# Kernel tuning notes

Measured on AMD Instinct MI355X. Metric: run time of the kernel, lower is better.

The kernel has to match this reference:

```python
import jax, jax.numpy as jnp
import numpy as np

N = 50000        # nodes
E = 800000       # edges (avg degree 16)
F = 64           # node_feature
H = 128          # dim_h
C = 10           # num_classes
G = 512          # graphs in batch
BN_EPS = 1e-5


def setup_inputs() -> dict:
    key = jax.random.key(0)
    ks = iter(jax.random.split(key, 40))
    inp = {}
    inp['x'] = jax.random.normal(next(ks), (N, F), dtype=jnp.float32)
    inp['edge_index'] = jax.random.randint(next(ks), (2, E), 0, N, dtype=jnp.int32)
    inp['batch'] = jnp.sort(jax.random.randint(next(ks), (N,), 0, G, dtype=jnp.int32))
    # GINConv MLP params (Linear, BatchNorm1d(eval), ReLU, Linear, ReLU) x3
    in_dims = [F, H, H]
    for i in range(1, 4):
        d_in = in_dims[i - 1]
        inp[f'c{i}_w1'] = jax.random.normal(next(ks), (d_in, H), dtype=jnp.float32) * 0.05
        inp[f'c{i}_b1'] = jnp.zeros((H,), dtype=jnp.float32)
        inp[f'c{i}_g'] = jnp.ones((H,), dtype=jnp.float32)
        inp[f'c{i}_be'] = jnp.zeros((H,), dtype=jnp.float32)
        inp[f'c{i}_m'] = jax.random.normal(next(ks), (H,), dtype=jnp.float32) * 0.01
        inp[f'c{i}_v'] = jax.random.uniform(next(ks), (H,), dtype=jnp.float32) + 0.5
        inp[f'c{i}_w2'] = jax.random.normal(next(ks), (H, H), dtype=jnp.float32) * 0.05
        inp[f'c{i}_b2'] = jnp.zeros((H,), dtype=jnp.float32)
    inp['lin1_w'] = jax.random.normal(next(ks), (3 * H, 3 * H), dtype=jnp.float32) * 0.05
    inp['lin1_b'] = jnp.zeros((3 * H,), dtype=jnp.float32)
    inp['lin2_w'] = jax.random.normal(next(ks), (3 * H, C), dtype=jnp.float32) * 0.05
    inp['lin2_b'] = jnp.zeros((C,), dtype=jnp.float32)
    return inp


def _mlp(h, w1, b1, g, be, m, v, w2, b2):
    h = h @ w1 + b1
    h = (h - m) * jax.lax.rsqrt(v + BN_EPS) * g + be  # BatchNorm1d (eval)
    h = jax.nn.relu(h)
    return jax.nn.relu(h @ w2 + b2)


def _gin_conv(x, src, dst, w1, b1, g, be, m, v, w2, b2):
    # GINConv, eps=0: MLP(x_i + sum_{j->i} x_j)
    agg = jax.ops.segment_sum(x[src], dst, num_segments=N)
    return _mlp(x + agg, w1, b1, g, be, m, v, w2, b2)


def reference(x, edge_index, batch,
              c1_w1, c1_b1, c1_g, c1_be, c1_m, c1_v, c1_w2, c1_b2,
              c2_w1, c2_b1, c2_g, c2_be, c2_m, c2_v, c2_w2, c2_b2,
              c3_w1, c3_b1, c3_g, c3_be, c3_m, c3_v, c3_w2, c3_b2,
              lin1_w, lin1_b, lin2_w, lin2_b):
    src, dst = edge_index[0], edge_index[1]
    h1 = _gin_conv(x, src, dst, c1_w1, c1_b1, c1_g, c1_be, c1_m, c1_v, c1_w2, c1_b2)
    h2 = _gin_conv(h1, src, dst, c2_w1, c2_b1, c2_g, c2_be, c2_m, c2_v, c2_w2, c2_b2)
    h3 = _gin_conv(h2, src, dst, c3_w1, c3_b1, c3_g, c3_be, c3_m, c3_v, c3_w2, c3_b2)
    p1 = jax.ops.segment_sum(h1, batch, num_segments=G)  # global_add_pool
    p2 = jax.ops.segment_sum(h2, batch, num_segments=G)
    p3 = jax.ops.segment_sum(h3, batch, num_segments=G)
    h = jnp.concatenate((p1, p2, p3), axis=1)  # [G, 3H]
    h = jax.nn.relu(h @ lin1_w + lin1_b)
    # dropout is identity in eval mode
    h = h @ lin2_w + lin2_b
    return jax.nn.log_softmax(h, axis=1)
```

## Files before the change

### kernel.cpp

```cpp
#include <hip/hip_runtime.h>
#include <math.h>
#include <stdint.h>

static constexpr int NN = 50000;
static constexpr int NE = 800000;
static constexpr int NG = 512;
static constexpr int NB = (NN + 255) / 256;
static constexpr float BNEPS = 1e-5f;

typedef __bf16 bf16x8 __attribute__((ext_vector_type(8)));
typedef __bf16 bf16x2 __attribute__((ext_vector_type(2)));
typedef float f32x4 __attribute__((ext_vector_type(4)));

__device__ __forceinline__ uint32_t pack_bf16(float x, float y) {
    bf16x2 v; v[0] = (__bf16)x; v[1] = (__bf16)y;
    return __builtin_bit_cast(uint32_t, v);
}
__device__ __forceinline__ float2 unpack_bf16(uint32_t u) {
    bf16x2 v = __builtin_bit_cast(bf16x2, u);
    return make_float2((float)v[0], (float)v[1]);
}


__global__ void degree_kernel(const int* __restrict__ dst, int* __restrict__ deg,
                              uint16_t* __restrict__ rank) {
    int e = blockIdx.x * blockDim.x + threadIdx.x;
    if (e < NE) rank[e] = (uint16_t)atomicAdd(&deg[dst[e]], 1);
}

__global__ __launch_bounds__(256) void blocksum_kernel(const int* __restrict__ deg,
                                                       int* __restrict__ bsum) {
    int i = blockIdx.x * 256 + threadIdx.x;
    int v = (i < NN) ? deg[i] : 0;
#pragma unroll
    for (int off = 32; off; off >>= 1) v += __shfl_down(v, off, 64);
    __shared__ int s[4];
    if ((threadIdx.x & 63) == 0) s[threadIdx.x >> 6] = v;
    __syncthreads();
    if (threadIdx.x == 0) bsum[blockIdx.x] = s[0] + s[1] + s[2] + s[3];
}

__global__ __launch_bounds__(256) void scanb_kernel(const int* __restrict__ bsum,
                                                    int* __restrict__ bscan,
                                                    int* __restrict__ row_ptr) {
    __shared__ int s[256];
    int t = threadIdx.x;
    int v = (t < NB) ? bsum[t] : 0;
    s[t] = v;
    __syncthreads();
    for (int off = 1; off < 256; off <<= 1) {
        int u = (t >= off) ? s[t - off] : 0;
        __syncthreads();
        s[t] += u;
        __syncthreads();
    }
    if (t < NB) bscan[t] = s[t] - v;
    if (t == NB - 1) row_ptr[NN] = s[t];
}

__global__ __launch_bounds__(256) void scanfinal_kernel(const int* __restrict__ deg,
                                                        const int* __restrict__ bscan,
                                                        int* __restrict__ row_ptr) {
    __shared__ int s[256];
    int t = threadIdx.x;
    int i = blockIdx.x * 256 + t;
    int v = (i < NN) ? deg[i] : 0;
    s[t] = v;
    __syncthreads();
    for (int off = 1; off < 256; off <<= 1) {
        int u = (t >= off) ? s[t - off] : 0;
        __syncthreads();
        s[t] += u;
        __syncthreads();
    }
    if (i < NN) row_ptr[i] = bscan[blockIdx.x] + s[t] - v;
}

__global__ void fill_kernel(const int* __restrict__ src, const int* __restrict__ dst,
                            const int* __restrict__ row_ptr, const uint16_t* __restrict__ rank,
                            uint16_t* __restrict__ cols) {
    int e = blockIdx.x * blockDim.x + threadIdx.x;
    if (e < NE) cols[row_ptr[dst[e]] + (int)rank[e]] = (uint16_t)src[e];
}


__global__ void prep_kernel(const float* __restrict__ x, __bf16* __restrict__ xb,
                            const float* s0, const float* s1, const float* s2,
                            const float* s3, const float* s4, const float* s5,
                            const float* s6,
                            __bf16* d0, __bf16* d1, __bf16* d2,
                            __bf16* d3, __bf16* d4, __bf16* d5, __bf16* d6) {
    int i = blockIdx.x * blockDim.x + threadIdx.x;
    if (i < 800000) {
        float4 v = *(const float4*)&x[i * 4];
        xb[i * 4 + 0] = (__bf16)v.x;
        xb[i * 4 + 1] = (__bf16)v.y;
        xb[i * 4 + 2] = (__bf16)v.z;
        xb[i * 4 + 3] = (__bf16)v.w;
        return;
    }
    int j = i - 800000;
    if (j < 8192) {
        int l = j;           int n = l / 64,  k = l % 64;  d0[l] = (__bf16)s0[k * 128 + n];
    } else if (j < 24576) {
        int l = j - 8192;    int n = l / 128, k = l % 128; d1[l] = (__bf16)s1[k * 128 + n];
    } else if (j < 40960) {
        int l = j - 24576;   int n = l / 128, k = l % 128; d2[l] = (__bf16)s2[k * 128 + n];
    } else if (j < 57344) {
        int l = j - 40960;   int n = l / 128, k = l % 128; d3[l] = (__bf16)s3[k * 128 + n];
    } else if (j < 73728) {
        int l = j - 57344;   int n = l / 128, k = l % 128; d4[l] = (__bf16)s4[k * 128 + n];
    } else if (j < 90112) {
        int l = j - 73728;   int n = l / 128, k = l % 128; d5[l] = (__bf16)s5[k * 128 + n];
    } else if (j < 237568) {
        int l = j - 90112;   int n = l / 384, k = l % 384; d6[l] = (__bf16)s6[k * 384 + n];
    }
}


__global__ __launch_bounds__(512) void gather64_kernel(const __bf16* __restrict__ in,
                                                       const int* __restrict__ row_ptr,
                                                       const uint16_t* __restrict__ cols,
                                                       __bf16* __restrict__ agg) {
    int node = blockIdx.x * 8 + (threadIdx.x >> 6);
    int lane = threadIdx.x & 63;
    if (node >= NN) return;
    int beg = row_ptr[node], end = row_ptr[node + 1];
    float acc0 = (float)in[(size_t)node * 64 + lane];
    float acc1 = 0.f;
    int i = beg;
    for (; i + 8 <= end; i += 8) {
        int c0 = cols[i], c1 = cols[i + 1], c2 = cols[i + 2], c3 = cols[i + 3];
        int c4 = cols[i + 4], c5 = cols[i + 5], c6 = cols[i + 6], c7 = cols[i + 7];
        float v0 = (float)in[(size_t)c0 * 64 + lane];
        float v1 = (float)in[(size_t)c1 * 64 + lane];
        float v2 = (float)in[(size_t)c2 * 64 + lane];
        float v3 = (float)in[(size_t)c3 * 64 + lane];
        float v4 = (float)in[(size_t)c4 * 64 + lane];
        float v5 = (float)in[(size_t)c5 * 64 + lane];
        float v6 = (float)in[(size_t)c6 * 64 + lane];
        float v7 = (float)in[(size_t)c7 * 64 + lane];
        acc0 += (v0 + v1) + (v2 + v3);
        acc1 += (v4 + v5) + (v6 + v7);
    }
    for (; i < end; ++i) acc0 += (float)in[(size_t)cols[i] * 64 + lane];
    agg[(size_t)node * 64 + lane] = (__bf16)(acc0 + acc1);
}

__global__ __launch_bounds__(512) void gather128_kernel(const __bf16* __restrict__ in,
                                                        const int* __restrict__ row_ptr,
                                                        const uint16_t* __restrict__ cols,
                                                        __bf16* __restrict__ agg) {
    int node = blockIdx.x * 8 + (threadIdx.x >> 6);
    int lane = threadIdx.x & 63;
    if (node >= NN) return;
    const uint32_t* inu = (const uint32_t*)in;
    uint32_t* aggu = (uint32_t*)agg;
    int beg = row_ptr[node], end = row_ptr[node + 1];
    float2 a0 = unpack_bf16(inu[(size_t)node * 64 + lane]);
    float2 a1 = make_float2(0.f, 0.f);
    int i = beg;
    for (; i + 8 <= end; i += 8) {
        int c0 = cols[i], c1 = cols[i + 1], c2 = cols[i + 2], c3 = cols[i + 3];
        int c4 = cols[i + 4], c5 = cols[i + 5], c6 = cols[i + 6], c7 = cols[i + 7];
        uint32_t u0 = inu[(size_t)c0 * 64 + lane];
        uint32_t u1 = inu[(size_t)c1 * 64 + lane];
        uint32_t u2 = inu[(size_t)c2 * 64 + lane];
        uint32_t u3 = inu[(size_t)c3 * 64 + lane];
        uint32_t u4 = inu[(size_t)c4 * 64 + lane];
        uint32_t u5 = inu[(size_t)c5 * 64 + lane];
        uint32_t u6 = inu[(size_t)c6 * 64 + lane];
        uint32_t u7 = inu[(size_t)c7 * 64 + lane];
        float2 v0 = unpack_bf16(u0), v1 = unpack_bf16(u1);
        float2 v2 = unpack_bf16(u2), v3 = unpack_bf16(u3);
        float2 v4 = unpack_bf16(u4), v5 = unpack_bf16(u5);
        float2 v6 = unpack_bf16(u6), v7 = unpack_bf16(u7);
        a0.x += (v0.x + v1.x) + (v2.x + v3.x);
        a0.y += (v0.y + v1.y) + (v2.y + v3.y);
        a1.x += (v4.x + v5.x) + (v6.x + v7.x);
        a1.y += (v4.y + v5.y) + (v6.y + v7.y);
    }
    for (; i < end; ++i) {
        float2 v = unpack_bf16(inu[(size_t)cols[i] * 64 + lane]);
        a0.x += v.x; a0.y += v.y;
    }
    aggu[(size_t)node * 64 + lane] = pack_bf16(a0.x + a1.x, a0.y + a1.y);
}


template <int K, bool WOUT>
__global__ __launch_bounds__(512, 1) void mlp_mfma_kernel(
    const __bf16* __restrict__ agg,
    const __bf16* __restrict__ w1t,
    const float* __restrict__ b1,
    const float* __restrict__ g, const float* __restrict__ be,
    const float* __restrict__ m, const float* __restrict__ v,
    const __bf16* __restrict__ w2t,
    const float* __restrict__ b2,
    __bf16* __restrict__ out,
    const int* __restrict__ batch,
    float* __restrict__ p,
    int col_off)
{
    constexpr int KP = K + 8;
    constexpr int KP2 = 136;
    __shared__ alignas(16) __bf16 sA[64 * KP];
    __shared__ alignas(16) __bf16 sW1[128 * KP];
    __shared__ alignas(16) __bf16 sW2[128 * KP2];
    __shared__ alignas(16) __bf16 sT[64 * KP2];
    __shared__ alignas(16) __bf16 sOut[64 * KP2];
    __shared__ int sBatch[64];

    int tid = threadIdx.x;
    int wid = tid >> 6, lane = tid & 63;
    int wr = wid >> 1, wc = wid & 1;
    int l15 = lane & 15, lq = lane >> 4;
    int rowbase = blockIdx.x * 64;

    for (int idx = tid; idx < 64 * (K / 8); idx += 512) {
        int r = idx / (K / 8), kc = idx % (K / 8);
        int n = rowbase + r;
        uint4 val = make_uint4(0, 0, 0, 0);
        if (n < NN) val = *(const uint4*)&agg[(size_t)n * K + kc * 8];
        *(uint4*)&sA[r * KP + kc * 8] = val;
    }
    for (int idx = tid; idx < 128 * (K / 8); idx += 512) {
        int n = idx / (K / 8), kc = idx % (K / 8);
        *(uint4*)&sW1[n * KP + kc * 8] = *(const uint4*)&w1t[n * K + kc * 8];
    }
    for (int idx = tid; idx < 128 * 16; idx += 512) {
        int n = idx >> 4, kc = idx & 15;
        *(uint4*)&sW2[n * KP2 + kc * 8] = *(const uint4*)&w2t[n * 128 + kc * 8];
    }
    if (tid < 64) {
        int n = rowbase + tid;
        sBatch[tid] = (n < NN) ? batch[n] : -1;
    }
    __syncthreads();

    f32x4 acc[4] = {};
#pragma unroll
    for (int ks = 0; ks < K / 32; ++ks) {
        bf16x8 a = *(const bf16x8*)&sA[(wr * 16 + l15) * KP + ks * 32 + lq * 8];
#pragma unroll
        for (int nf = 0; nf < 4; ++nf) {
            bf16x8 b = *(const bf16x8*)&sW1[(wc * 64 + nf * 16 + l15) * KP + ks * 32 + lq * 8];
            acc[nf] = __builtin_amdgcn_mfma_f32_16x16x32_bf16(a, b, acc[nf], 0, 0, 0);
        }
    }
#pragma unroll
    for (int nf = 0; nf < 4; ++nf) {
        int c = wc * 64 + nf * 16 + l15;
        float sc = g[c] * rsqrtf(v[c] + BNEPS);
        float sh = be[c] + (b1[c] - m[c]) * sc;
#pragma unroll
        for (int r = 0; r < 4; ++r) {
            int row = wr * 16 + lq * 4 + r;
            float t = fmaxf(acc[nf][r] * sc + sh, 0.f);
            sT[row * KP2 + c] = (__bf16)t;
        }
    }
    __syncthreads();

    f32x4 acc2[4] = {};
#pragma unroll
    for (int ks = 0; ks < 4; ++ks) {
        bf16x8 a = *(const bf16x8*)&sT[(wr * 16 + l15) * KP2 + ks * 32 + lq * 8];
#pragma unroll
        for (int nf = 0; nf < 4; ++nf) {
            bf16x8 b = *(const bf16x8*)&sW2[(wc * 64 + nf * 16 + l15) * KP2 + ks * 32 + lq * 8];
            acc2[nf] = __builtin_amdgcn_mfma_f32_16x16x32_bf16(a, b, acc2[nf], 0, 0, 0);
        }
    }
#pragma unroll
    for (int nf = 0; nf < 4; ++nf) {
        int c = wc * 64 + nf * 16 + l15;
        float bb = b2[c];
#pragma unroll
        for (int r = 0; r < 4; ++r) {
            int row = wr * 16 + lq * 4 + r;
            float o = fmaxf(acc2[nf][r] + bb, 0.f);
            sOut[row * KP2 + c] = (__bf16)o;
        }
    }
    __syncthreads();

    if constexpr (WOUT) {
        for (int idx = tid; idx < 64 * 16; idx += 512) {
            int r = idx >> 4, kc = idx & 15;
            int n = rowbase + r;
            if (n < NN)
                *(uint4*)&out[(size_t)n * 128 + kc * 8] = *(const uint4*)&sOut[r * KP2 + kc * 8];
        }
    }

    {
        int f = tid & 127;
        int chunk = tid >> 7;
        float pacc = 0.f;
        int cur = -1;
#pragma unroll
        for (int i = 0; i < 16; ++i) {
            int row = chunk * 16 + i;
            int b = sBatch[row];
            if (b < 0) break;
            if (b != cur) {
                if (cur >= 0) atomicAdd(&p[cur * 384 + col_off + f], pacc);
                pacc = 0.f;
                cur = b;
            }
            pacc += (float)sOut[row * KP2 + f];
        }
        if (cur >= 0) atomicAdd(&p[cur * 384 + col_off + f], pacc);
    }
}


__global__ __launch_bounds__(512, 1) void head1_kernel(const float* __restrict__ p,
                                                       const __bf16* __restrict__ lin1t,
                                                       const float* __restrict__ b1,
                                                       float* __restrict__ hrelu) {
    constexpr int KPA = 392;
    constexpr int KPW = 136;
    __shared__ alignas(16) __bf16 sA[64 * KPA];
    __shared__ alignas(16) __bf16 sW[128 * KPW];

    int tid = threadIdx.x;
    int wid = tid >> 6, lane = tid & 63;
    int wr = wid >> 1, wc = wid & 1;
    int l15 = lane & 15, lq = lane >> 4;
    int rowbase = blockIdx.x * 64;
    int colbase = blockIdx.y * 128;

    for (int idx = tid; idx < 64 * 48; idx += 512) {
        int r = idx / 48, kc = idx % 48;
        const float* srcp = &p[(rowbase + r) * 384 + kc * 8];
        float4 v0 = *(const float4*)srcp;
        float4 v1 = *(const float4*)(srcp + 4);
        bf16x8 o;
        o[0] = (__bf16)v0.x; o[1] = (__bf16)v0.y; o[2] = (__bf16)v0.z; o[3] = (__bf16)v0.w;
        o[4] = (__bf16)v1.x; o[5] = (__bf16)v1.y; o[6] = (__bf16)v1.z; o[7] = (__bf16)v1.w;
        *(bf16x8*)&sA[r * KPA + kc * 8] = o;
    }

    f32x4 acc[4] = {};
#pragma unroll
    for (int kchunk = 0; kchunk < 3; ++kchunk) {
        for (int idx = tid; idx < 128 * 16; idx += 512) {
            int n = idx >> 4, kc = idx & 15;
            *(uint4*)&sW[n * KPW + kc * 8] =
                *(const uint4*)&lin1t[(colbase + n) * 384 + kchunk * 128 + kc * 8];
        }
        __syncthreads();
#pragma unroll
        for (int ks = 0; ks < 4; ++ks) {
            bf16x8 a = *(const bf16x8*)&sA[(wr * 16 + l15) * KPA + kchunk * 128 + ks * 32 + lq * 8];
#pragma unroll
            for (int nf = 0; nf < 4; ++nf) {
                bf16x8 b = *(const bf16x8*)&sW[(wc * 64 + nf * 16 + l15) * KPW + ks * 32 + lq * 8];
                acc[nf] = __builtin_amdgcn_mfma_f32_16x16x32_bf16(a, b, acc[nf], 0, 0, 0);
            }
        }
        __syncthreads();
    }
#pragma unroll
    for (int nf = 0; nf < 4; ++nf) {
        int col = colbase + wc * 64 + nf * 16 + l15;
        float bb = b1[col];
#pragma unroll
        for (int r = 0; r < 4; ++r) {
            int row = rowbase + wr * 16 + lq * 4 + r;
            hrelu[row * 384 + col] = fmaxf(acc[nf][r] + bb, 0.f);
        }
    }
}


__global__ __launch_bounds__(256) void head2_kernel(const float* __restrict__ hrelu,
                                                    const float* __restrict__ w2,
                                                    const float* __restrict__ b2,
                                                    float* __restrict__ out) {
    int wid = threadIdx.x >> 6, lane = threadIdx.x & 63;
    int gidx = blockIdx.x * 4 + wid;
    const float* hr = &hrelu[gidx * 384 + lane * 6];
    float h[6];
#pragma unroll
    for (int u = 0; u < 6; ++u) h[u] = hr[u];
    float logit[10];
#pragma unroll
    for (int c = 0; c < 10; ++c) {
        float s = 0.f;
#pragma unroll
        for (int u = 0; u < 6; ++u) s = fmaf(h[u], w2[(lane * 6 + u) * 10 + c], s);
#pragma unroll
        for (int off = 32; off; off >>= 1) s += __shfl_xor(s, off, 64);
        logit[c] = s + b2[c];
    }
    float mx = logit[0];
#pragma unroll
    for (int c = 1; c < 10; ++c) mx = fmaxf(mx, logit[c]);
    float se = 0.f;
#pragma unroll
    for (int c = 0; c < 10; ++c) se += expf(logit[c] - mx);
    float lse = logf(se);
    float val = 0.f;
#pragma unroll
    for (int c = 0; c < 10; ++c) if (lane == c) val = logit[c];
    if (lane < 10) out[gidx * 10 + lane] = val - mx - lse;
}


static inline char* align_up(char* ptr, size_t a) {
    return (char*)(((uintptr_t)ptr + a - 1) & ~(uintptr_t)(a - 1));
}

extern "C" void kernel_launch(void* const* d_in, const int* in_sizes, int n_in,
                              void* d_out, int out_size, void* d_ws, size_t ws_size,
                              hipStream_t stream) {
    const float* x = (const float*)d_in[0];
    const int* ei = (const int*)d_in[1];
    const int* batch = (const int*)d_in[2];
    const float* c_w1[3], *c_b1[3], *c_g[3], *c_be[3], *c_m[3], *c_v[3], *c_w2[3], *c_b2[3];
    for (int i = 0; i < 3; ++i) {
        int base = 3 + i * 8;
        c_w1[i] = (const float*)d_in[base + 0];
        c_b1[i] = (const float*)d_in[base + 1];
        c_g[i]  = (const float*)d_in[base + 2];
        c_be[i] = (const float*)d_in[base + 3];
        c_m[i]  = (const float*)d_in[base + 4];
        c_v[i]  = (const float*)d_in[base + 5];
        c_w2[i] = (const float*)d_in[base + 6];
        c_b2[i] = (const float*)d_in[base + 7];
    }
    const float* lin1_w = (const float*)d_in[27];
    const float* lin1_b = (const float*)d_in[28];
    const float* lin2_w = (const float*)d_in[29];
    const float* lin2_b = (const float*)d_in[30];
    const int* src = ei;
    const int* dst = ei + NE;
    float* out = (float*)d_out;

    char* ws = (char*)d_ws;
    __bf16* xb  = (__bf16*)ws; ws = align_up(ws + (size_t)NN * 64 * 2, 256);
    __bf16* agg = (__bf16*)ws; ws = align_up(ws + (size_t)NN * 128 * 2, 256);
    __bf16* hA  = (__bf16*)ws; ws = align_up(ws + (size_t)NN * 128 * 2, 256);
    __bf16* hB  = (__bf16*)ws; ws = align_up(ws + (size_t)NN * 128 * 2, 256);
    float* p    = (float*)ws;  ws = align_up(ws + (size_t)NG * 384 * 4, 256);
    float* hrelu = (float*)ws; ws = align_up(ws + (size_t)NG * 384 * 4, 256);
    int* csr_row = (int*)ws;   ws = align_up(ws + (size_t)(NN + 1) * 4, 256);
    int* cursor  = (int*)ws;   ws = align_up(ws + (size_t)NN * 4, 256);
    uint16_t* csr_src = (uint16_t*)ws; ws = align_up(ws + (size_t)NE * 2, 256);
    uint16_t* rank    = (uint16_t*)ws; ws = align_up(ws + (size_t)NE * 2, 256);
    int* bsum    = (int*)ws;   ws = align_up(ws + (size_t)NB * 4, 256);
    int* bscan   = (int*)ws;   ws = align_up(ws + (size_t)NB * 4, 256);
    __bf16* w1t[3]; __bf16* w2t[3];
    for (int i = 0; i < 3; ++i) {
        int K = (i == 0) ? 64 : 128;
        w1t[i] = (__bf16*)ws; ws = align_up(ws + (size_t)128 * K * 2, 256);
        w2t[i] = (__bf16*)ws; ws = align_up(ws + (size_t)128 * 128 * 2, 256);
    }
    __bf16* lin1t = (__bf16*)ws; ws = align_up(ws + (size_t)384 * 384 * 2, 256);

    hipMemsetAsync(cursor, 0, (size_t)NN * 4, stream);
    degree_kernel<<<(NE + 255) / 256, 256, 0, stream>>>(dst, cursor, rank);
    blocksum_kernel<<<NB, 256, 0, stream>>>(cursor, bsum);
    scanb_kernel<<<1, 256, 0, stream>>>(bsum, bscan, csr_row);
    scanfinal_kernel<<<NB, 256, 0, stream>>>(cursor, bscan, csr_row);
    fill_kernel<<<(NE + 255) / 256, 256, 0, stream>>>(src, dst, csr_row, rank, csr_src);
    hipMemsetAsync(p, 0, (size_t)NG * 384 * 4, stream);

    prep_kernel<<<(800000 + 237568 + 255) / 256, 256, 0, stream>>>(
        x, xb,
        c_w1[0], c_w1[1], c_w1[2], c_w2[0], c_w2[1], c_w2[2], lin1_w,
        w1t[0], w1t[1], w1t[2], w2t[0], w2t[1], w2t[2], lin1t);

    const int GATHER_BLOCKS = (NN + 7) / 8;
    const int MLP_BLOCKS = (NN + 63) / 64;

    gather64_kernel<<<GATHER_BLOCKS, 512, 0, stream>>>(xb, csr_row, csr_src, agg);
    mlp_mfma_kernel<64, true><<<MLP_BLOCKS, 512, 0, stream>>>(agg, w1t[0], c_b1[0], c_g[0], c_be[0],
                                                              c_m[0], c_v[0], w2t[0], c_b2[0], hA,
                                                              batch, p, 0);

    gather128_kernel<<<GATHER_BLOCKS, 512, 0, stream>>>(hA, csr_row, csr_src, agg);
    mlp_mfma_kernel<128, true><<<MLP_BLOCKS, 512, 0, stream>>>(agg, w1t[1], c_b1[1], c_g[1], c_be[1],
                                                               c_m[1], c_v[1], w2t[1], c_b2[1], hB,
                                                               batch, p, 128);

    gather128_kernel<<<GATHER_BLOCKS, 512, 0, stream>>>(hB, csr_row, csr_src, agg);
    mlp_mfma_kernel<128, false><<<MLP_BLOCKS, 512, 0, stream>>>(agg, w1t[2], c_b1[2], c_g[2], c_be[2],
                                                                c_m[2], c_v[2], w2t[2], c_b2[2], nullptr,
                                                                batch, p, 256);

    head1_kernel<<<dim3(8, 3), 512, 0, stream>>>(p, lin1t, lin1_b, hrelu);
    head2_kernel<<<128, 256, 0, stream>>>(hrelu, lin2_w, lin2_b, out);
}
```

Measured before the change: 273.2 us.

## Split gather into column passes with 16-lane groups per node

Replaces the per-wave-per-node gather kernels with one templated kernel. Each 16-lane subgroup handles one node and a 64-byte column slice, and blockIdx.y selects which slice. The intent is to shrink the working set of source rows touched at once so it fits in cache better, and to fit more nodes per wave, which cuts wasted lanes on low-degree nodes. In exchange, the CSR row pointers and column indices are reread once per column pass, the accesses are narrower, and the inner loop is unrolled 4 instead of 8, so fewer loads are in flight.

```diff
diff --git a/kernel.cpp b/kernel.cpp
--- a/kernel.cpp
+++ b/kernel.cpp
@@ -118,73 +118,39 @@
 }
 
 
-__global__ __launch_bounds__(512) void gather64_kernel(const __bf16* __restrict__ in,
-                                                       const int* __restrict__ row_ptr,
-                                                       const uint16_t* __restrict__ cols,
-                                                       __bf16* __restrict__ agg) {
-    int node = blockIdx.x * 8 + (threadIdx.x >> 6);
-    int lane = threadIdx.x & 63;
+template <int DWPR>
+__global__ __launch_bounds__(512) void gather_pass_kernel(const __bf16* __restrict__ in,
+                                                          const int* __restrict__ row_ptr,
+                                                          const uint16_t* __restrict__ cols,
+                                                          __bf16* __restrict__ agg) {
+    int wid = threadIdx.x >> 6;
+    int sub = (threadIdx.x & 63) >> 4;
+    int l16 = threadIdx.x & 15;
+    int node = (blockIdx.x * 8 + wid) * 4 + sub;
     if (node >= NN) return;
-    int beg = row_ptr[node], end = row_ptr[node + 1];
-    float acc0 = (float)in[(size_t)node * 64 + lane];
-    float acc1 = 0.f;
-    int i = beg;
-    for (; i + 8 <= end; i += 8) {
-        int c0 = cols[i], c1 = cols[i + 1], c2 = cols[i + 2], c3 = cols[i + 3];
-        int c4 = cols[i + 4], c5 = cols[i + 5], c6 = cols[i + 6], c7 = cols[i + 7];
-        float v0 = (float)in[(size_t)c0 * 64 + lane];
-        float v1 = (float)in[(size_t)c1 * 64 + lane];
-        float v2 = (float)in[(size_t)c2 * 64 + lane];
-        float v3 = (float)in[(size_t)c3 * 64 + lane];
-        float v4 = (float)in[(size_t)c4 * 64 + lane];
-        float v5 = (float)in[(size_t)c5 * 64 + lane];
-        float v6 = (float)in[(size_t)c6 * 64 + lane];
-        float v7 = (float)in[(size_t)c7 * 64 + lane];
-        acc0 += (v0 + v1) + (v2 + v3);
-        acc1 += (v4 + v5) + (v6 + v7);
-    }
-    for (; i < end; ++i) acc0 += (float)in[(size_t)cols[i] * 64 + lane];
-    agg[(size_t)node * 64 + lane] = (__bf16)(acc0 + acc1);
-}
-
-__global__ __launch_bounds__(512) void gather128_kernel(const __bf16* __restrict__ in,
-                                                        const int* __restrict__ row_ptr,
-                                                        const uint16_t* __restrict__ cols,
-                                                        __bf16* __restrict__ agg) {
-    int node = blockIdx.x * 8 + (threadIdx.x >> 6);
-    int lane = threadIdx.x & 63;
-    if (node >= NN) return;
+    int off = blockIdx.y * 16 + l16;
     const uint32_t* inu = (const uint32_t*)in;
     uint32_t* aggu = (uint32_t*)agg;
     int beg = row_ptr[node], end = row_ptr[node + 1];
-    float2 a0 = unpack_bf16(inu[(size_t)node * 64 + lane]);
+    float2 a0 = unpack_bf16(inu[(size_t)node * DWPR + off]);
     float2 a1 = make_float2(0.f, 0.f);
     int i = beg;
-    for (; i + 8 <= end; i += 8) {
+    for (; i + 4 <= end; i += 4) {
         int c0 = cols[i], c1 = cols[i + 1], c2 = cols[i + 2], c3 = cols[i + 3];
-        int c4 = cols[i + 4], c5 = cols[i + 5], c6 = cols[i + 6], c7 = cols[i + 7];
-        uint32_t u0 = inu[(size_t)c0 * 64 + lane];
-        uint32_t u1 = inu[(size_t)c1 * 64 + lane];
-        uint32_t u2 = inu[(size_t)c2 * 64 + lane];
-        uint32_t u3 = inu[(size_t)c3 * 64 + lane];
-        uint32_t u4 = inu[(size_t)c4 * 64 + lane];
-        uint32_t u5 = inu[(size_t)c5 * 64 + lane];
-        uint32_t u6 = inu[(size_t)c6 * 64 + lane];
-        uint32_t u7 = inu[(size_t)c7 * 64 + lane];
+        uint32_t u0 = inu[(size_t)c0 * DWPR + off];
+        uint32_t u1 = inu[(size_t)c1 * DWPR + off];
+        uint32_t u2 = inu[(size_t)c2 * DWPR + off];
+        uint32_t u3 = inu[(size_t)c3 * DWPR + off];
         float2 v0 = unpack_bf16(u0), v1 = unpack_bf16(u1);
         float2 v2 = unpack_bf16(u2), v3 = unpack_bf16(u3);
-        float2 v4 = unpack_bf16(u4), v5 = unpack_bf16(u5);
-        float2 v6 = unpack_bf16(u6), v7 = unpack_bf16(u7);
-        a0.x += (v0.x + v1.x) + (v2.x + v3.x);
-        a0.y += (v0.y + v1.y) + (v2.y + v3.y);
-        a1.x += (v4.x + v5.x) + (v6.x + v7.x);
-        a1.y += (v4.y + v5.y) + (v6.y + v7.y);
+        a0.x += v0.x + v1.x; a0.y += v0.y + v1.y;
+        a1.x += v2.x + v3.x; a1.y += v2.y + v3.y;
     }
     for (; i < end; ++i) {
-        float2 v = unpack_bf16(inu[(size_t)cols[i] * 64 + lane]);
+        float2 v = unpack_bf16(inu[(size_t)cols[i] * DWPR + off]);
         a0.x += v.x; a0.y += v.y;
     }
-    aggu[(size_t)node * 64 + lane] = pack_bf16(a0.x + a1.x, a0.y + a1.y);
+    aggu[(size_t)node * DWPR + off] = pack_bf16(a0.x + a1.x, a0.y + a1.y);
 }
 
 
@@ -474,20 +440,20 @@
         c_w1[0], c_w1[1], c_w1[2], c_w2[0], c_w2[1], c_w2[2], lin1_w,
         w1t[0], w1t[1], w1t[2], w2t[0], w2t[1], w2t[2], lin1t);
 
-    const int GATHER_BLOCKS = (NN + 7) / 8;
+    const int GATHER_X = (NN + 31) / 32;
     const int MLP_BLOCKS = (NN + 63) / 64;
 
-    gather64_kernel<<<GATHER_BLOCKS, 512, 0, stream>>>(xb, csr_row, csr_src, agg);
+    gather_pass_kernel<32><<<dim3(GATHER_X, 2), 512, 0, stream>>>(xb, csr_row, csr_src, agg);
     mlp_mfma_kernel<64, true><<<MLP_BLOCKS, 512, 0, stream>>>(agg, w1t[0], c_b1[0], c_g[0], c_be[0],
                                                               c_m[0], c_v[0], w2t[0], c_b2[0], hA,
                                                               batch, p, 0);
 
-    gather128_kernel<<<GATHER_BLOCKS, 512, 0, stream>>>(hA, csr_row, csr_src, agg);
+    gather_pass_kernel<64><<<dim3(GATHER_X, 4), 512, 0, stream>>>(hA, csr_row, csr_src, agg);
     mlp_mfma_kernel<128, true><<<MLP_BLOCKS, 512, 0, stream>>>(agg, w1t[1], c_b1[1], c_g[1], c_be[1],
                                                                c_m[1], c_v[1], w2t[1], c_b2[1], hB,
                                                                batch, p, 128);
 
-    gather128_kernel<<<GATHER_BLOCKS, 512, 0, stream>>>(hB, csr_row, csr_src, agg);
+    gather_pass_kernel<64><<<dim3(GATHER_X, 4), 512, 0, stream>>>(hB, csr_row, csr_src, agg);
     mlp_mfma_kernel<128, false><<<MLP_BLOCKS, 512, 0, stream>>>(agg, w1t[2], c_b1[2], c_g[2], c_be[2],
                                                                 c_m[2], c_v[2], w2t[2], c_b2[2], nullptr,
                                                                 batch, p, 256);
```

After: 288.1 us. 1.05x slower.
